# Performance work log

Measured on AMD Instinct MI355X. Metric: run time of the kernel, lower is better.

Reference implementation:

```python
import math
import jax, jax.numpy as jnp
import numpy as np

WS = 4            # window size
LS = 2 * WS       # local context size
NH = 8            # num heads
DIM = 128
EPS = 1e-5


def setup_inputs() -> dict:
    key = jax.random.key(0)
    ks = jax.random.split(key, 8)
    B, C, H, W = 4, DIM, 48, 48
    features = jax.random.normal(ks[0], (B, C, H, W), dtype=jnp.float32)
    s = 0.02
    return {
        'features': features,
        'ln_w': jnp.ones((C,), jnp.float32),
        'ln_b': jnp.zeros((C,), jnp.float32),
        'q_w': jax.random.normal(ks[1], (C, C), jnp.float32) * s,
        'q_b': jnp.zeros((C,), jnp.float32),
        'kv_w': jax.random.normal(ks[2], (2 * C, C), jnp.float32) * s,
        'kv_b': jnp.zeros((2 * C,), jnp.float32),
        'out_w': jax.random.normal(ks[3], (C, C), jnp.float32) * s,
        'out_b': jnp.zeros((C,), jnp.float32),
    }


def _avgpool_tokens(x, k):
    # x: [B,C,H,W] -> [B, (H//k)*(W//k), C]
    B, C, H, W = x.shape
    t = x.reshape(B, C, H // k, k, W // k, k).mean(axis=(3, 5))
    return t.reshape(B, C, -1).transpose(0, 2, 1)


def reference(features, ln_w, ln_b, q_w, q_b, kv_w, kv_b, out_w, out_b):
    B, C, H, W = features.shape
    Hw, Ww = H // WS, W // WS
    nw = Hw * Ww
    hd = C // NH

    # ---- window partition: [B,C,H,W] -> [B*nw, WS*WS, C]
    qt = features.reshape(B, C, Hw, WS, Ww, WS).transpose(0, 2, 4, 3, 5, 1)
    qt = qt.reshape(B * nw, WS * WS, C)

    # ---- LayerNorm(dim)
    mu = qt.mean(-1, keepdims=True)
    var = qt.var(-1, keepdims=True)
    qt = (qt - mu) / jnp.sqrt(var + EPS) * ln_w + ln_b

    # ---- local context: pad to target, unfold kernel=LS stride=WS
    target = (int(math.sqrt(nw)) - 1) * WS + LS
    ph, pw = max(0, target - H), max(0, target - W)
    pad = ((0, 0), (0, 0), (ph // 2, ph - ph // 2), (pw // 2, pw - pw // 2))
    padded = jnp.pad(features, pad)
    # channel order of patches is (C, kh, kw), same as torch unfold
    patches = jax.lax.conv_general_dilated_patches(
        padded, filter_shape=(LS, LS), window_strides=(WS, WS), padding='VALID')
    local = patches.reshape(B, C, LS * LS, nw).transpose(0, 3, 2, 1)
    local = local.reshape(B * nw, LS * LS, C)

    # ---- multi-scale pooled tokens, broadcast to each window
    mid = _avgpool_tokens(features, 2)      # [B, M, C]
    glo = _avgpool_tokens(features, 4)      # [B, G, C]
    mid = jnp.broadcast_to(mid[:, None], (B, nw) + mid.shape[1:]).reshape(B * nw, -1, C)
    glo = jnp.broadcast_to(glo[:, None], (B, nw) + glo.shape[1:]).reshape(B * nw, -1, C)

    kv_tokens = jnp.concatenate([local, mid, glo], axis=1)  # [B*nw, Nkv, C]

    # ---- projections (torch Linear: x @ W.T + b)
    queries = qt @ q_w.T + q_b
    kv = kv_tokens @ kv_w.T + kv_b
    keys, values = kv[..., :C], kv[..., C:]

    # ---- multi-head attention
    Nq, Nkv = queries.shape[1], keys.shape[1]
    q = queries.reshape(-1, Nq, NH, hd)
    k = keys.reshape(-1, Nkv, NH, hd)
    v = values.reshape(-1, Nkv, NH, hd)
    scores = jnp.einsum('bqhd,bkhd->bhqk', q, k) / math.sqrt(hd)
    weights = jax.nn.softmax(scores, axis=-1)
    attended = jnp.einsum('bhqk,bkhd->bqhd', weights, v).reshape(-1, Nq, C)

    out = attended @ out_w.T + out_b

    # ---- window reconstruction -> [B,C,H,W]
    out = out.reshape(B, Hw, Ww, WS, WS, C).transpose(0, 5, 1, 3, 2, 4)
    out = out.reshape(B, C, H, W)
    return out + features
```

## Files before the change

kernel.cpp:

```cpp
#include <hip/hip_runtime.h>


typedef unsigned short u16;
typedef short v8s __attribute__((ext_vector_type(8)));
typedef v8s __attribute__((may_alias)) v8s_am;
typedef short v4s __attribute__((ext_vector_type(4)));
typedef v4s __attribute__((may_alias)) v4s_am;
typedef float v4f __attribute__((ext_vector_type(4)));

#define MFMA_BF16(a, b, c) __builtin_amdgcn_mfma_f32_16x16x32_bf16(a, b, c, 0, 0, 0)

#if __has_builtin(__builtin_amdgcn_mfma_f32_16x16x16bf16_1k)
#define MFMA16(a, b, c) __builtin_amdgcn_mfma_f32_16x16x16bf16_1k(a, b, c, 0, 0, 0)
#else
static __device__ __forceinline__ v4f mfma16_fb(v4s a, v4s b, v4f c) {
    v8s a8 = {a[0], a[1], a[2], a[3], 0, 0, 0, 0};
    v8s b8 = {b[0], b[1], b[2], b[3], 0, 0, 0, 0};
    return MFMA_BF16(a8, b8, c);
}
#define MFMA16(a, b, c) mfma16_fb(a, b, c)
#endif

#if __has_builtin(__builtin_amdgcn_exp2f)
#define EXP2(x) __builtin_amdgcn_exp2f(x)
#else
#define EXP2(x) exp2f(x)
#endif

__device__ __forceinline__ float b2f(u16 u) {
    union { unsigned int i; float f; } x;
    x.i = ((unsigned int)u) << 16;
    return x.f;
}
__device__ __forceinline__ u16 f2b(float f) {
    union { float f; unsigned int i; } x;
    x.f = f;
    unsigned int u = x.i;
    return (u16)((u + 0x7fffu + ((u >> 16) & 1u)) >> 16);
}

__global__ __launch_bounds__(256) void k_prep(
    const float* __restrict__ F,
    const float* __restrict__ qw, const float* __restrict__ kvw,
    const float* __restrict__ ow,
    const float* __restrict__ lnw, const float* __restrict__ lnb,
    u16* __restrict__ Xt, u16* __restrict__ Wb, float* __restrict__ MuRs,
    u16* __restrict__ Pml)
{
    int blk = blockIdx.x;
    int t = threadIdx.x;
    if (blk >= 304) {
        int gid = (blk - 304) * 256 + t;
        int row = gid >> 4;
        int seg = gid & 15;
        v8s outv;
        if (row < 2304) {
            int b = row / 576, r = row % 576;
            int i = r / 24, j = r % 24;
#pragma unroll
            for (int jc = 0; jc < 8; ++jc) {
                int c = seg * 8 + jc;
                const float* src = F + ((size_t)(b * 128 + c)) * 2304 + (2 * i) * 48 + 2 * j;
                float2 a = *(const float2*)src;
                float2 d = *(const float2*)(src + 48);
                outv[jc] = (short)f2b((a.x + a.y + d.x + d.y) * 0.25f);
            }
        } else {
            int r2 = row - 2304;
            int b = r2 / 144, r = r2 % 144;
            int i = r / 12, j = r % 12;
#pragma unroll
            for (int jc = 0; jc < 8; ++jc) {
                int c = seg * 8 + jc;
                const float* src = F + ((size_t)(b * 128 + c)) * 2304 + (4 * i) * 48 + 4 * j;
                float s = 0.f;
#pragma unroll
                for (int di = 0; di < 4; ++di) {
                    float4 v = *(const float4*)(src + di * 48);
                    s += (v.x + v.y) + (v.z + v.w);
                }
                outv[jc] = (short)f2b(s * 0.0625f);
            }
        }
        *(v8s_am*)&Pml[((size_t)row) * 128 + seg * 8] = outv;
        return;
    }
    if (blk >= 288) {
        int base = (blk - 288) * 4096 + t * 16;
#pragma unroll
        for (int i = 0; i < 4; ++i) {
            int idx = base + i * 4;
            const float* src; int off;
            if (idx < 16384)      { src = qw;  off = idx; }
            else if (idx < 49152) { src = kvw; off = idx - 16384; }
            else                  { src = ow;  off = idx - 49152; }
            float4 v = *(const float4*)(src + off);
            unsigned long long packed =
                (unsigned long long)f2b(v.x) |
                ((unsigned long long)f2b(v.y) << 16) |
                ((unsigned long long)f2b(v.z) << 32) |
                ((unsigned long long)f2b(v.w) << 48);
            *(unsigned long long*)(Wb + idx) = packed;
        }
        if (blk == 288) {
            Wb[65536 + t] = f2b(t < 128 ? lnw[t] : lnb[t - 128]);
        }
        return;
    }
    __shared__ u16 X[128][34];
    int b = blk / 72;
    int p0 = (blk % 72) * 32;
#pragma unroll 4
    for (int i = 0; i < 16; ++i) {
        int c = i * 8 + (t >> 5);
        int pix = t & 31;
        X[c][pix] = f2b(F[((size_t)(b * 128 + c)) * 2304 + p0 + pix]);
    }
    __syncthreads();
    int pix = t >> 3;
    int c0 = (t & 7) * 16;
    size_t row = (size_t)(b * 2304 + p0 + pix) * 128;
    float s = 0.f, s2 = 0.f;
#pragma unroll
    for (int sg = 0; sg < 2; ++sg) {
        v8s raw;
#pragma unroll
        for (int j = 0; j < 8; ++j) {
            u16 u = X[c0 + sg * 8 + j][pix];
            raw[j] = (short)u;
            float v = b2f(u);
            s += v; s2 += v * v;
        }
        *(v8s_am*)&Xt[row + c0 + sg * 8] = raw;
    }
    s += __shfl_xor(s, 1);  s2 += __shfl_xor(s2, 1);
    s += __shfl_xor(s, 2);  s2 += __shfl_xor(s2, 2);
    s += __shfl_xor(s, 4);  s2 += __shfl_xor(s2, 4);
    if ((t & 7) == 0) {
        float mean = s * (1.f / 128.f);
        float var = s2 * (1.f / 128.f) - mean * mean;
        float rstd = rsqrtf(var + 1e-5f);
        MuRs[(b * 2304 + p0 + pix) * 2]     = mean;
        MuRs[(b * 2304 + p0 + pix) * 2 + 1] = rstd;
    }
}

__global__ __launch_bounds__(256) void k_gemm_kv(
    const u16* __restrict__ Pml,
    const u16* __restrict__ W,
    const float* __restrict__ bias,
    u16* __restrict__ KVg,
    u16* __restrict__ VTg)
{
    __shared__ u16 Al[64][136];
    __shared__ u16 Wl[64][136];
    int tm = blockIdx.x * 64, tn = blockIdx.y * 64;
    int t = threadIdx.x;
    {
        int seg = t & 15, r0 = t >> 4;
#pragma unroll
        for (int i = 0; i < 4; ++i) {
            int r = r0 + 16 * i;
            *(v8s_am*)&Al[r][seg * 8] = *(const v8s_am*)&Pml[((size_t)(tm + r)) * 128 + seg * 8];
            *(v8s_am*)&Wl[r][seg * 8] = *(const v8s_am*)&W[((size_t)(tn + r)) * 128 + seg * 8];
        }
    }
    __syncthreads();
    int lane = t & 63, wave = t >> 6;
    int n15 = lane & 15, quad = lane >> 4;
    int wm = (wave & 1) * 32, wn = (wave >> 1) * 32;
    v4f acc[2][2] = {};
#pragma unroll
    for (int kc = 0; kc < 4; ++kc) {
        v8s a[2], bb[2];
#pragma unroll
        for (int im = 0; im < 2; ++im)
            a[im] = *(const v8s_am*)&Al[wm + im * 16 + n15][kc * 32 + quad * 8];
#pragma unroll
        for (int in = 0; in < 2; ++in)
            bb[in] = *(const v8s_am*)&Wl[wn + in * 16 + n15][kc * 32 + quad * 8];
#pragma unroll
        for (int im = 0; im < 2; ++im)
#pragma unroll
            for (int in = 0; in < 2; ++in)
                acc[im][in] = MFMA_BF16(a[im], bb[in], acc[im][in]);
    }
#pragma unroll
    for (int in = 0; in < 2; ++in) {
        int n = tn + wn + in * 16 + n15;
        float bv = bias[n];
#pragma unroll
        for (int im = 0; im < 2; ++im) {
            int mbase = tm + wm + im * 16 + quad * 4;
#pragma unroll
            for (int r = 0; r < 4; ++r) {
                int m = mbase + r;
                u16 h = f2b(acc[im][in][r] + bv);
                if (n < 128) {
                    KVg[((size_t)m) * 128 + n] = h;
                } else {
                    int ch = n - 128, bb2, tok;
                    if (m < 2304) { bb2 = m / 576; tok = m % 576; }
                    else { int r2 = m - 2304; bb2 = r2 / 144; tok = 576 + r2 % 144; }
                    VTg[((size_t)(bb2 * 128 + ch)) * 720 + tok] = h;
                }
            }
        }
    }
}

__global__ __launch_bounds__(512, 4) void k_attn_fused(
    const float* __restrict__ F,
    const u16* __restrict__ Xt,
    const float* __restrict__ MuRs,
    const u16* __restrict__ KVg,
    const u16* __restrict__ VTg,
    const u16* __restrict__ Wb,
    const float* __restrict__ qb,
    const float* __restrict__ kvb,
    const float* __restrict__ ob,
    float* __restrict__ Out)
{
    __shared__ u16 KB[2][64][136];
    __shared__ u16 VtW[8][16][68];

    const u16* qwb  = Wb;
    const u16* kvwb = Wb + 16384;
    const u16* owb  = Wb + 49152;
    const u16* lnwb = Wb + 65536;
    const u16* lnbb = Wb + 65664;
    u16* Atp = &VtW[0][0][0];

    int blk = blockIdx.x;
    int xcd = blk & 7, jj = blk >> 3;
    int b = xcd >> 1;
    int wr = (xcd & 1) * 6 + jj / 12;
    int wc = jj % 12;

    int t = threadIdx.x;
    int lane = t & 63, wave = t >> 6, n15 = lane & 15, quad = lane >> 4;
    v8s zf8 = {};
    v4f zz4 = {0.f, 0.f, 0.f, 0.f};
    const float QSCALE = 0.25f * 1.44269504f;

    int qh = wr * 4 + (n15 >> 2), qw_ = wc * 4 + (n15 & 3);
    int qpix = b * 2304 + qh * 48 + qw_;
    float mu = MuRs[qpix * 2], rstd = MuRs[qpix * 2 + 1];
    v8s xln[4];
#pragma unroll
    for (int kc = 0; kc < 4; ++kc) {
        v8s x  = *(const v8s_am*)&Xt[(size_t)qpix * 128 + kc * 32 + quad * 8];
        v8s lw = *(const v8s_am*)&lnwb[kc * 32 + quad * 8];
        v8s lb = *(const v8s_am*)&lnbb[kc * 32 + quad * 8];
        v8s y;
#pragma unroll
        for (int j = 0; j < 8; ++j)
            y[j] = (short)f2b((b2f((u16)x[j]) - mu) * rstd * b2f((u16)lw[j]) + b2f((u16)lb[j]));
        xln[kc] = y;
    }

    v4s qf;
    {
        int n0 = wave * 16;
        v4f qacc = zz4;
#pragma unroll
        for (int kc = 0; kc < 4; ++kc) {
            v8s aw = *(const v8s_am*)&qwb[((size_t)(n0 + n15)) * 128 + kc * 32 + quad * 8];
            qacc = MFMA_BF16(aw, xln[kc], qacc);
        }
#pragma unroll
        for (int r = 0; r < 4; ++r)
            qf[r] = (short)f2b((qacc[r] + qb[n0 + quad * 4 + r]) * QSCALE);
    }

    v4s kfloc[4];
#pragma unroll
    for (int g = 0; g < 4; ++g) {
        int tl = g * 16 + n15;
        int fh = tl >> 3, fw = tl & 7;
        int hh = wr * 4 - 2 + fh, ww = wc * 4 - 2 + fw;
        bool valid = (hh >= 0 && hh < 48 && ww >= 0 && ww < 48);
        size_t arow = (size_t)(b * 2304 + hh * 48 + ww) * 128;
        v8s xb[4];
#pragma unroll
        for (int kc = 0; kc < 4; ++kc) {
            v8s v = zf8;
            if (valid) v = *(const v8s_am*)&Xt[arow + kc * 32 + quad * 8];
            xb[kc] = v;
        }
#pragma unroll
        for (int s = 0; s < 2; ++s) {
            int sbase = s * 128 + wave * 16;
            v4f acc = zz4;
#pragma unroll
            for (int kc = 0; kc < 4; ++kc) {
                v8s aw = *(const v8s_am*)&kvwb[((size_t)(sbase + n15)) * 128 + kc * 32 + quad * 8];
                acc = MFMA_BF16(aw, xb[kc], acc);
            }
            if (s == 0) {
                v4s k4;
#pragma unroll
                for (int r = 0; r < 4; ++r)
                    k4[r] = (short)f2b(acc[r] + kvb[sbase + quad * 4 + r]);
                kfloc[g] = k4;
            } else {
#pragma unroll
                for (int r = 0; r < 4; ++r)
                    VtW[wave][quad * 4 + r][g * 16 + n15] =
                        f2b(acc[r] + kvb[sbase + quad * 4 + r]);
            }
        }
    }

    v8s stg[2];
#pragma unroll
    for (int i = 0; i < 2; ++i) {
        int chunk = i * 512 + t;
        stg[i] = *(const v8s_am*)&KVg[((size_t)(b * 576 + (chunk >> 4))) * 128 + (chunk & 15) * 8];
    }

    v4f oacc = zz4;
    float ls = 0.f;
    const u16* VTb = VTg + (size_t)b * 92160;

    asm volatile("s_waitcnt lgkmcnt(0)" ::: "memory");
#pragma unroll
    for (int g = 0; g < 4; ++g) {
        v4f St = MFMA16(kfloc[g], qf, zz4);
        float p0 = EXP2(St[0]), p1 = EXP2(St[1]);
        float p2 = EXP2(St[2]), p3 = EXP2(St[3]);
        ls += (p0 + p1) + (p2 + p3);
        v4s pk = {(short)f2b(p0), (short)f2b(p1), (short)f2b(p2), (short)f2b(p3)};
        v4s vf = *(const v4s_am*)&VtW[wave][n15][g * 16 + quad * 4];
        oacc = MFMA16(vf, pk, oacc);
    }

#pragma unroll
    for (int i = 0; i < 2; ++i) {
        int chunk = i * 512 + t;
        *(v8s_am*)&KB[1][chunk >> 4][(chunk & 15) * 8] = stg[i];
    }
    __syncthreads();

    for (int tb = 0; tb <= 10; ++tb) {
        v4s vp[4];
        {
            const u16* vrow = VTb + (size_t)(wave * 16 + n15) * 720 + tb * 64 + quad * 4;
#pragma unroll
            for (int g = 0; g < 4; ++g)
                vp[g] = *(const v4s_am*)(vrow + g * 16);
        }
        int nt_ = tb + 1;
        int rowbase = (nt_ < 9) ? (b * 576 + nt_ * 64)
                                : (2304 + b * 144 + nt_ * 64 - 576);
        int nrows = (nt_ == 11) ? 16 : 64;
        bool sv[2];
#pragma unroll
        for (int i = 0; i < 2; ++i) {
            int chunk = i * 512 + t;
            int rr = chunk >> 4;
            sv[i] = rr < nrows;
            if (sv[i])
                stg[i] = *(const v8s_am*)&KVg[((size_t)(rowbase + rr)) * 128 + (chunk & 15) * 8];
        }
        const u16 (*KBc)[136] = KB[1 - (tb & 1)];
#pragma unroll
        for (int g = 0; g < 4; ++g) {
            v4s kf = *(const v4s_am*)&KBc[g * 16 + n15][wave * 16 + quad * 4];
            v4f St = MFMA16(kf, qf, zz4);
            float p0 = EXP2(St[0]), p1 = EXP2(St[1]);
            float p2 = EXP2(St[2]), p3 = EXP2(St[3]);
            ls += (p0 + p1) + (p2 + p3);
            v4s pk = {(short)f2b(p0), (short)f2b(p1), (short)f2b(p2), (short)f2b(p3)};
            oacc = MFMA16(vp[g], pk, oacc);
        }
#pragma unroll
        for (int i = 0; i < 2; ++i) {
            if (sv[i]) {
                int chunk = i * 512 + t;
                *(v8s_am*)&KB[tb & 1][chunk >> 4][(chunk & 15) * 8] = stg[i];
            }
        }
        __syncthreads();
    }
    {
        v4s vf = *(const v4s_am*)(VTb + (size_t)(wave * 16 + n15) * 720 + 704 + quad * 4);
        v4s kf = *(const v4s_am*)&KB[0][n15][wave * 16 + quad * 4];
        v4f St = MFMA16(kf, qf, zz4);
        float p0 = EXP2(St[0]), p1 = EXP2(St[1]);
        float p2 = EXP2(St[2]), p3 = EXP2(St[3]);
        ls += (p0 + p1) + (p2 + p3);
        v4s pk = {(short)f2b(p0), (short)f2b(p1), (short)f2b(p2), (short)f2b(p3)};
        oacc = MFMA16(vf, pk, oacc);
    }

    ls += __shfl_xor(ls, 16);
    ls += __shfl_xor(ls, 32);
    {
        float inv = 1.f / ls;
        v4s a4 = {(short)f2b(oacc[0] * inv), (short)f2b(oacc[1] * inv),
                  (short)f2b(oacc[2] * inv), (short)f2b(oacc[3] * inv)};
        *(v4s_am*)&Atp[n15 * 136 + wave * 16 + quad * 4] = a4;
    }
    __syncthreads();

    {
        int n0 = wave * 16;
        v4f oa = zz4;
#pragma unroll
        for (int kc = 0; kc < 4; ++kc) {
            v8s af = *(const v8s_am*)&Atp[n15 * 136 + kc * 32 + quad * 8];
            v8s bf = *(const v8s_am*)&owb[((size_t)(n0 + n15)) * 128 + kc * 32 + quad * 8];
            oa = MFMA_BF16(af, bf, oa);
        }
        int c = n0 + n15;
        float bv = ob[c];
#pragma unroll
        for (int r = 0; r < 4; ++r) {
            int pix = quad * 4 + r;
            int hh = wr * 4 + (pix >> 2), ww_ = wc * 4 + (pix & 3);
            size_t idx = ((size_t)(b * 128 + c)) * 2304 + hh * 48 + ww_;
            Out[idx] = oa[r] + bv + F[idx];
        }
    }
}

extern "C" void kernel_launch(void* const* d_in, const int* in_sizes, int n_in,
                              void* d_out, int out_size, void* d_ws, size_t ws_size,
                              hipStream_t stream)
{
    const float* F   = (const float*)d_in[0];
    const float* lnw = (const float*)d_in[1];
    const float* lnb = (const float*)d_in[2];
    const float* qw  = (const float*)d_in[3];
    const float* qb  = (const float*)d_in[4];
    const float* kvw = (const float*)d_in[5];
    const float* kvb = (const float*)d_in[6];
    const float* ow  = (const float*)d_in[7];
    const float* ob  = (const float*)d_in[8];
    float* Out = (float*)d_out;

    u16* ws    = (u16*)d_ws;
    u16* Xt    = ws;
    u16* Pml   = Xt + 9216 * 128;
    u16* KVg   = Pml + 2880 * 128;
    u16* VTg   = KVg + 2880 * 128;
    u16* Wb    = VTg + 4 * 128 * 720;
    float* MuRs = (float*)(Wb + 65792);
    u16* kvwb = Wb + 16384;

    k_prep<<<484, 256, 0, stream>>>(F, qw, kvw, ow, lnw, lnb, Xt, Wb, MuRs, Pml);
    k_gemm_kv<<<dim3(45, 4), 256, 0, stream>>>(Pml, kvwb, kvb, KVg, VTg);
    k_attn_fused<<<576, 512, 0, stream>>>(F, Xt, MuRs, KVg, VTg, Wb,
                                          qb, kvb, ob, Out);
}
```

Baseline: 135.1 us.

## Fuse pooling into KV GEMM, stage V transpose via LDS, drop K LDS buffering

The average pooling of mid/global tokens moves out of the prep kernel and into the KV GEMM, which reads the bf16 transposed features (Xt) instead of a separate pooled buffer, so one kernel's work and one intermediate round trip go away. V outputs of the mid-scale tiles are transposed through LDS so VTg gets vectorised, coalesced stores. The attention kernel stops double-buffering K tiles in shared memory with per-tile barriers and instead loads K and V fragments straight from global memory, which lowers LDS use and removes syncs but adds strided global loads that depend on cache hits. Pooling now runs on bf16-rounded features, which can change numerics slightly.

```diff
diff --git a/kernel.cpp b/kernel.cpp
--- a/kernel.cpp
+++ b/kernel.cpp
@@ -44,47 +44,10 @@
     const float* __restrict__ qw, const float* __restrict__ kvw,
     const float* __restrict__ ow,
     const float* __restrict__ lnw, const float* __restrict__ lnb,
-    u16* __restrict__ Xt, u16* __restrict__ Wb, float* __restrict__ MuRs,
-    u16* __restrict__ Pml)
+    u16* __restrict__ Xt, u16* __restrict__ Wb, float* __restrict__ MuRs)
 {
     int blk = blockIdx.x;
     int t = threadIdx.x;
-    if (blk >= 304) {
-        int gid = (blk - 304) * 256 + t;
-        int row = gid >> 4;
-        int seg = gid & 15;
-        v8s outv;
-        if (row < 2304) {
-            int b = row / 576, r = row % 576;
-            int i = r / 24, j = r % 24;
-#pragma unroll
-            for (int jc = 0; jc < 8; ++jc) {
-                int c = seg * 8 + jc;
-                const float* src = F + ((size_t)(b * 128 + c)) * 2304 + (2 * i) * 48 + 2 * j;
-                float2 a = *(const float2*)src;
-                float2 d = *(const float2*)(src + 48);
-                outv[jc] = (short)f2b((a.x + a.y + d.x + d.y) * 0.25f);
-            }
-        } else {
-            int r2 = row - 2304;
-            int b = r2 / 144, r = r2 % 144;
-            int i = r / 12, j = r % 12;
-#pragma unroll
-            for (int jc = 0; jc < 8; ++jc) {
-                int c = seg * 8 + jc;
-                const float* src = F + ((size_t)(b * 128 + c)) * 2304 + (4 * i) * 48 + 4 * j;
-                float s = 0.f;
-#pragma unroll
-                for (int di = 0; di < 4; ++di) {
-                    float4 v = *(const float4*)(src + di * 48);
-                    s += (v.x + v.y) + (v.z + v.w);
-                }
-                outv[jc] = (short)f2b(s * 0.0625f);
-            }
-        }
-        *(v8s_am*)&Pml[((size_t)row) * 128 + seg * 8] = outv;
-        return;
-    }
     if (blk >= 288) {
         int base = (blk - 288) * 4096 + t * 16;
 #pragma unroll
@@ -146,7 +109,7 @@
 }
 
 __global__ __launch_bounds__(256) void k_gemm_kv(
-    const u16* __restrict__ Pml,
+    const u16* __restrict__ Xt,
     const u16* __restrict__ W,
     const float* __restrict__ bias,
     u16* __restrict__ KVg,
@@ -161,8 +124,59 @@
 #pragma unroll
         for (int i = 0; i < 4; ++i) {
             int r = r0 + 16 * i;
-            *(v8s_am*)&Al[r][seg * 8] = *(const v8s_am*)&Pml[((size_t)(tm + r)) * 128 + seg * 8];
             *(v8s_am*)&Wl[r][seg * 8] = *(const v8s_am*)&W[((size_t)(tn + r)) * 128 + seg * 8];
+        }
+    }
+    {
+        int r = t >> 2;
+        int cp = (t & 3) * 32;
+        int m = tm + r;
+        float s[32];
+#pragma unroll
+        for (int j = 0; j < 32; ++j) s[j] = 0.f;
+        if (m < 2304) {
+            int b = m / 576, loc = m % 576;
+            int i = loc / 24, j = loc % 24;
+            int base = b * 2304 + (2 * i) * 48 + 2 * j;
+#pragma unroll
+            for (int rr = 0; rr < 4; ++rr) {
+                int row = base + (rr >> 1) * 48 + (rr & 1);
+#pragma unroll
+                for (int k = 0; k < 4; ++k) {
+                    v8s x = *(const v8s_am*)&Xt[(size_t)row * 128 + cp + k * 8];
+#pragma unroll
+                    for (int jj = 0; jj < 8; ++jj) s[k * 8 + jj] += b2f((u16)x[jj]);
+                }
+            }
+#pragma unroll
+            for (int k = 0; k < 4; ++k) {
+                v8s o;
+#pragma unroll
+                for (int jj = 0; jj < 8; ++jj) o[jj] = (short)f2b(s[k * 8 + jj] * 0.25f);
+                *(v8s_am*)&Al[r][cp + k * 8] = o;
+            }
+        } else {
+            int r2 = m - 2304;
+            int b = r2 / 144, loc = r2 % 144;
+            int i = loc / 12, j = loc % 12;
+            int base = b * 2304 + (4 * i) * 48 + 4 * j;
+#pragma unroll
+            for (int rr = 0; rr < 16; ++rr) {
+                int row = base + (rr >> 2) * 48 + (rr & 3);
+#pragma unroll
+                for (int k = 0; k < 4; ++k) {
+                    v8s x = *(const v8s_am*)&Xt[(size_t)row * 128 + cp + k * 8];
+#pragma unroll
+                    for (int jj = 0; jj < 8; ++jj) s[k * 8 + jj] += b2f((u16)x[jj]);
+                }
+            }
+#pragma unroll
+            for (int k = 0; k < 4; ++k) {
+                v8s o;
+#pragma unroll
+                for (int jj = 0; jj < 8; ++jj) o[jj] = (short)f2b(s[k * 8 + jj] * 0.0625f);
+                *(v8s_am*)&Al[r][cp + k * 8] = o;
+            }
         }
     }
     __syncthreads();
@@ -185,6 +199,10 @@
             for (int in = 0; in < 2; ++in)
                 acc[im][in] = MFMA_BF16(a[im], bb[in], acc[im][in]);
     }
+    bool vblk = (tn >= 128);
+    bool vfast = vblk && (tm < 2304);
+    u16* vt = &Al[0][0];
+    if (vfast) __syncthreads();
 #pragma unroll
     for (int in = 0; in < 2; ++in) {
         int n = tn + wn + in * 16 + n15;
@@ -196,17 +214,32 @@
             for (int r = 0; r < 4; ++r) {
                 int m = mbase + r;
                 u16 h = f2b(acc[im][in][r] + bv);
-                if (n < 128) {
+                if (!vblk) {
                     KVg[((size_t)m) * 128 + n] = h;
+                } else if (vfast) {
+                    vt[(n - tn) * 72 + (wm + im * 16 + quad * 4 + r)] = h;
                 } else {
                     int ch = n - 128, bb2, tok;
-                    if (m < 2304) { bb2 = m / 576; tok = m % 576; }
-                    else { int r2 = m - 2304; bb2 = r2 / 144; tok = 576 + r2 % 144; }
+                    int r2 = m - 2304; bb2 = r2 / 144; tok = 576 + r2 % 144;
                     VTg[((size_t)(bb2 * 128 + ch)) * 720 + tok] = h;
                 }
             }
         }
     }
+    if (vfast) {
+        __syncthreads();
+        int ch = t >> 2, seg = t & 3;
+        int b = tm / 576, tokbase = tm % 576;
+        v8s a0 = *(const v8s_am*)&vt[ch * 72 + seg * 16];
+        v8s a1 = *(const v8s_am*)&vt[ch * 72 + seg * 16 + 8];
+        size_t d = ((size_t)(b * 128 + (tn - 128) + ch)) * 720 + tokbase + seg * 16;
+        *(v8s_am*)&VTg[d]     = a0;
+        *(v8s_am*)&VTg[d + 8] = a1;
+    }
+}
+
+__device__ __forceinline__ int rbase_of(int b, int tb) {
+    return (tb < 9) ? (b * 576 + tb * 64) : (2304 + b * 144 + (tb - 9) * 64);
 }
 
 __global__ __launch_bounds__(512, 4) void k_attn_fused(
@@ -221,15 +254,14 @@
     const float* __restrict__ ob,
     float* __restrict__ Out)
 {
-    __shared__ u16 KB[2][64][136];
     __shared__ u16 VtW[8][16][68];
+    __shared__ u16 At[16][136];
 
     const u16* qwb  = Wb;
     const u16* kvwb = Wb + 16384;
     const u16* owb  = Wb + 49152;
     const u16* lnwb = Wb + 65536;
     const u16* lnbb = Wb + 65664;
-    u16* Atp = &VtW[0][0][0];
 
     int blk = blockIdx.x;
     int xcd = blk & 7, jj = blk >> 3;
@@ -312,18 +344,11 @@
         }
     }
 
-    v8s stg[2];
-#pragma unroll
-    for (int i = 0; i < 2; ++i) {
-        int chunk = i * 512 + t;
-        stg[i] = *(const v8s_am*)&KVg[((size_t)(b * 576 + (chunk >> 4))) * 128 + (chunk & 15) * 8];
-    }
-
     v4f oacc = zz4;
     float ls = 0.f;
-    const u16* VTb = VTg + (size_t)b * 92160;
 
     asm volatile("s_waitcnt lgkmcnt(0)" ::: "memory");
+    __builtin_amdgcn_sched_barrier(0);
 #pragma unroll
     for (int g = 0; g < 4; ++g) {
         v4f St = MFMA16(kfloc[g], qf, zz4);
@@ -335,57 +360,31 @@
         oacc = MFMA16(vf, pk, oacc);
     }
 
-#pragma unroll
-    for (int i = 0; i < 2; ++i) {
-        int chunk = i * 512 + t;
-        *(v8s_am*)&KB[1][chunk >> 4][(chunk & 15) * 8] = stg[i];
-    }
-    __syncthreads();
-
-    for (int tb = 0; tb <= 10; ++tb) {
-        v4s vp[4];
-        {
-            const u16* vrow = VTb + (size_t)(wave * 16 + n15) * 720 + tb * 64 + quad * 4;
-#pragma unroll
-            for (int g = 0; g < 4; ++g)
-                vp[g] = *(const v4s_am*)(vrow + g * 16);
-        }
-        int nt_ = tb + 1;
-        int rowbase = (nt_ < 9) ? (b * 576 + nt_ * 64)
-                                : (2304 + b * 144 + nt_ * 64 - 576);
-        int nrows = (nt_ == 11) ? 16 : 64;
-        bool sv[2];
-#pragma unroll
-        for (int i = 0; i < 2; ++i) {
-            int chunk = i * 512 + t;
-            int rr = chunk >> 4;
-            sv[i] = rr < nrows;
-            if (sv[i])
-                stg[i] = *(const v8s_am*)&KVg[((size_t)(rowbase + rr)) * 128 + (chunk & 15) * 8];
-        }
-        const u16 (*KBc)[136] = KB[1 - (tb & 1)];
+    const u16* kcol  = KVg + wave * 16 + quad * 4;
+    const u16* vrow0 = VTg + (size_t)b * 92160 + (size_t)(wave * 16 + n15) * 720 + quad * 4;
+#pragma unroll
+    for (int tb = 0; tb < 11; ++tb) {
+        int rbase = rbase_of(b, tb);
+        v4s kf[4], vp[4];
 #pragma unroll
         for (int g = 0; g < 4; ++g) {
-            v4s kf = *(const v4s_am*)&KBc[g * 16 + n15][wave * 16 + quad * 4];
-            v4f St = MFMA16(kf, qf, zz4);
+            kf[g] = *(const v4s_am*)(kcol + (size_t)(rbase + g * 16 + n15) * 128);
+            vp[g] = *(const v4s_am*)(vrow0 + tb * 64 + g * 16);
+        }
+#pragma unroll
+        for (int g = 0; g < 4; ++g) {
+            v4f St = MFMA16(kf[g], qf, zz4);
             float p0 = EXP2(St[0]), p1 = EXP2(St[1]);
             float p2 = EXP2(St[2]), p3 = EXP2(St[3]);
             ls += (p0 + p1) + (p2 + p3);
             v4s pk = {(short)f2b(p0), (short)f2b(p1), (short)f2b(p2), (short)f2b(p3)};
             oacc = MFMA16(vp[g], pk, oacc);
         }
-#pragma unroll
-        for (int i = 0; i < 2; ++i) {
-            if (sv[i]) {
-                int chunk = i * 512 + t;
-                *(v8s_am*)&KB[tb & 1][chunk >> 4][(chunk & 15) * 8] = stg[i];
-            }
-        }
-        __syncthreads();
-    }
-    {
-        v4s vf = *(const v4s_am*)(VTb + (size_t)(wave * 16 + n15) * 720 + 704 + quad * 4);
-        v4s kf = *(const v4s_am*)&KB[0][n15][wave * 16 + quad * 4];
+    }
+    {
+        int rbase = 2304 + b * 144 + 128;
+        v4s kf = *(const v4s_am*)(kcol + (size_t)(rbase + n15) * 128);
+        v4s vf = *(const v4s_am*)(vrow0 + 704);
         v4f St = MFMA16(kf, qf, zz4);
         float p0 = EXP2(St[0]), p1 = EXP2(St[1]);
         float p2 = EXP2(St[2]), p3 = EXP2(St[3]);
@@ -400,7 +399,7 @@
         float inv = 1.f / ls;
         v4s a4 = {(short)f2b(oacc[0] * inv), (short)f2b(oacc[1] * inv),
                   (short)f2b(oacc[2] * inv), (short)f2b(oacc[3] * inv)};
-        *(v4s_am*)&Atp[n15 * 136 + wave * 16 + quad * 4] = a4;
+        *(v4s_am*)&At[n15][wave * 16 + quad * 4] = a4;
     }
     __syncthreads();
 
@@ -409,7 +408,7 @@
         v4f oa = zz4;
 #pragma unroll
         for (int kc = 0; kc < 4; ++kc) {
-            v8s af = *(const v8s_am*)&Atp[n15 * 136 + kc * 32 + quad * 8];
+            v8s af = *(const v8s_am*)&At[n15][kc * 32 + quad * 8];
             v8s bf = *(const v8s_am*)&owb[((size_t)(n0 + n15)) * 128 + kc * 32 + quad * 8];
             oa = MFMA_BF16(af, bf, oa);
         }
@@ -449,8 +448,8 @@
     float* MuRs = (float*)(Wb + 65792);
     u16* kvwb = Wb + 16384;
 
-    k_prep<<<484, 256, 0, stream>>>(F, qw, kvw, ow, lnw, lnb, Xt, Wb, MuRs, Pml);
-    k_gemm_kv<<<dim3(45, 4), 256, 0, stream>>>(Pml, kvwb, kvb, KVg, VTg);
+    k_prep<<<304, 256, 0, stream>>>(F, qw, kvw, ow, lnw, lnb, Xt, Wb, MuRs);
+    k_gemm_kv<<<dim3(45, 4), 256, 0, stream>>>(Xt, kvwb, kvb, KVg, VTg);
     k_attn_fused<<<576, 512, 0, stream>>>(F, Xt, MuRs, KVg, VTg, Wb,
                                           qb, kvb, ob, Out);
 }
```

Result: slower. 151.6 us (+12.2%).

## Fuse pooling into KV GEMM prep kernel and process two windows per attention block

Applied to the files above, without the earlier changes.

Merges the pooled-token computation and the KV projection GEMM into the prep kernel. The GEMM blocks now pool features directly into shared memory and convert kv weights on the fly, which removes the Pml round trip and one launch. V-transpose writes for the mid tokens are staged through LDS so they go out as coalesced stores. The attention kernel now handles two adjacent windows per block (288 blocks), so each loaded shared K/V tile serves two query sets, at the cost of more registers and fewer blocks.

```diff
diff --git a/kernel.cpp b/kernel.cpp
--- a/kernel.cpp
+++ b/kernel.cpp
@@ -39,50 +39,136 @@
     return (u16)((u + 0x7fffu + ((u >> 16) & 1u)) >> 16);
 }
 
-__global__ __launch_bounds__(256) void k_prep(
+__global__ __launch_bounds__(256) void k_prep_gemm(
     const float* __restrict__ F,
     const float* __restrict__ qw, const float* __restrict__ kvw,
     const float* __restrict__ ow,
     const float* __restrict__ lnw, const float* __restrict__ lnb,
+    const float* __restrict__ kvb,
     u16* __restrict__ Xt, u16* __restrict__ Wb, float* __restrict__ MuRs,
-    u16* __restrict__ Pml)
+    u16* __restrict__ KVg, u16* __restrict__ VTg)
 {
+    __shared__ u16 SH[17408];
     int blk = blockIdx.x;
     int t = threadIdx.x;
+
     if (blk >= 304) {
-        int gid = (blk - 304) * 256 + t;
-        int row = gid >> 4;
-        int seg = gid & 15;
-        v8s outv;
-        if (row < 2304) {
-            int b = row / 576, r = row % 576;
-            int i = r / 24, j = r % 24;
-#pragma unroll
-            for (int jc = 0; jc < 8; ++jc) {
-                int c = seg * 8 + jc;
-                const float* src = F + ((size_t)(b * 128 + c)) * 2304 + (2 * i) * 48 + 2 * j;
-                float2 a = *(const float2*)src;
-                float2 d = *(const float2*)(src + 48);
-                outv[jc] = (short)f2b((a.x + a.y + d.x + d.y) * 0.25f);
-            }
-        } else {
-            int r2 = row - 2304;
-            int b = r2 / 144, r = r2 % 144;
-            int i = r / 12, j = r % 12;
-#pragma unroll
-            for (int jc = 0; jc < 8; ++jc) {
-                int c = seg * 8 + jc;
-                const float* src = F + ((size_t)(b * 128 + c)) * 2304 + (4 * i) * 48 + 4 * j;
-                float s = 0.f;
-#pragma unroll
-                for (int di = 0; di < 4; ++di) {
-                    float4 v = *(const float4*)(src + di * 48);
-                    s += (v.x + v.y) + (v.z + v.w);
+        u16 (*Al)[136] = (u16(*)[136])SH;
+        u16 (*Wl)[136] = (u16(*)[136])(SH + 8704);
+        int gb = blk - 304;
+        int tm = (gb % 45) * 64, tn = (gb / 45) * 64;
+        {
+            int seg = t & 15, r0 = t >> 4;
+#pragma unroll
+            for (int i = 0; i < 4; ++i) {
+                int r = r0 + 16 * i;
+                const float* src = kvw + (size_t)(tn + r) * 128 + seg * 8;
+                float4 v0 = *(const float4*)src;
+                float4 v1 = *(const float4*)(src + 4);
+                v8s o = {(short)f2b(v0.x), (short)f2b(v0.y), (short)f2b(v0.z), (short)f2b(v0.w),
+                         (short)f2b(v1.x), (short)f2b(v1.y), (short)f2b(v1.z), (short)f2b(v1.w)};
+                *(v8s_am*)&Wl[r][seg * 8] = o;
+            }
+        }
+        {
+            int rs = t >> 2;
+            int cp = (t & 3) * 32;
+            int m = tm + rs;
+            float s[32];
+            if (m < 2304) {
+                int bb = m / 576, loc = m % 576;
+                int ii = loc / 24, jj2 = loc % 24;
+                const float* f0 = F + (size_t)(bb * 128 + cp) * 2304 + (2 * ii) * 48 + 2 * jj2;
+#pragma unroll
+                for (int cc = 0; cc < 32; ++cc) {
+                    const float* src = f0 + (size_t)cc * 2304;
+                    float2 a = *(const float2*)src;
+                    float2 d = *(const float2*)(src + 48);
+                    s[cc] = (a.x + a.y + d.x + d.y) * 0.25f;
                 }
-                outv[jc] = (short)f2b(s * 0.0625f);
-            }
-        }
-        *(v8s_am*)&Pml[((size_t)row) * 128 + seg * 8] = outv;
+            } else {
+                int r2 = m - 2304;
+                int bb = r2 / 144, loc = r2 % 144;
+                int ii = loc / 12, jj2 = loc % 12;
+                const float* f0 = F + (size_t)(bb * 128 + cp) * 2304 + (4 * ii) * 48 + 4 * jj2;
+#pragma unroll
+                for (int cc = 0; cc < 32; ++cc) {
+                    const float* src = f0 + (size_t)cc * 2304;
+                    float ss = 0.f;
+#pragma unroll
+                    for (int di = 0; di < 4; ++di) {
+                        float4 v = *(const float4*)(src + di * 48);
+                        ss += (v.x + v.y) + (v.z + v.w);
+                    }
+                    s[cc] = ss * 0.0625f;
+                }
+            }
+#pragma unroll
+            for (int k = 0; k < 4; ++k) {
+                v8s o;
+#pragma unroll
+                for (int jj = 0; jj < 8; ++jj) o[jj] = (short)f2b(s[k * 8 + jj]);
+                *(v8s_am*)&Al[rs][cp + k * 8] = o;
+            }
+        }
+        __syncthreads();
+        int lane = t & 63, wave = t >> 6;
+        int n15 = lane & 15, quad = lane >> 4;
+        int wm = (wave & 1) * 32, wn = (wave >> 1) * 32;
+        v4f acc[2][2] = {};
+#pragma unroll
+        for (int kc = 0; kc < 4; ++kc) {
+            v8s a[2], bb[2];
+#pragma unroll
+            for (int im = 0; im < 2; ++im)
+                a[im] = *(const v8s_am*)&Al[wm + im * 16 + n15][kc * 32 + quad * 8];
+#pragma unroll
+            for (int in = 0; in < 2; ++in)
+                bb[in] = *(const v8s_am*)&Wl[wn + in * 16 + n15][kc * 32 + quad * 8];
+#pragma unroll
+            for (int im = 0; im < 2; ++im)
+#pragma unroll
+                for (int in = 0; in < 2; ++in)
+                    acc[im][in] = MFMA_BF16(a[im], bb[in], acc[im][in]);
+        }
+        bool vblk = (tn >= 128);
+        bool vfast = vblk && (tm < 2304);
+        u16* vt = &Al[0][0];
+        if (vfast) __syncthreads();
+#pragma unroll
+        for (int in = 0; in < 2; ++in) {
+            int n = tn + wn + in * 16 + n15;
+            float bv = kvb[n];
+#pragma unroll
+            for (int im = 0; im < 2; ++im) {
+                int mbase = tm + wm + im * 16 + quad * 4;
+#pragma unroll
+                for (int r = 0; r < 4; ++r) {
+                    int m = mbase + r;
+                    u16 h = f2b(acc[im][in][r] + bv);
+                    if (!vblk) {
+                        KVg[((size_t)m) * 128 + n] = h;
+                    } else if (vfast) {
+                        vt[(n - tn) * 72 + (wm + im * 16 + quad * 4 + r)] = h;
+                    } else {
+                        int ch = n - 128;
+                        int r2 = m - 2304;
+                        int bb2 = r2 / 144, tok = 576 + r2 % 144;
+                        VTg[((size_t)(bb2 * 128 + ch)) * 720 + tok] = h;
+                    }
+                }
+            }
+        }
+        if (vfast) {
+            __syncthreads();
+            int ch = t >> 2, seg = t & 3;
+            int bb2 = tm / 576, tokbase = tm % 576;
+            v8s a0 = *(const v8s_am*)&vt[ch * 72 + seg * 16];
+            v8s a1 = *(const v8s_am*)&vt[ch * 72 + seg * 16 + 8];
+            size_t d = ((size_t)(bb2 * 128 + (tn - 128) + ch)) * 720 + tokbase + seg * 16;
+            *(v8s_am*)&VTg[d]     = a0;
+            *(v8s_am*)&VTg[d + 8] = a1;
+        }
         return;
     }
     if (blk >= 288) {
@@ -107,7 +193,7 @@
         }
         return;
     }
-    __shared__ u16 X[128][34];
+    u16 (*X)[34] = (u16(*)[34])SH;
     int b = blk / 72;
     int p0 = (blk % 72) * 32;
 #pragma unroll 4
@@ -142,70 +228,6 @@
         float rstd = rsqrtf(var + 1e-5f);
         MuRs[(b * 2304 + p0 + pix) * 2]     = mean;
         MuRs[(b * 2304 + p0 + pix) * 2 + 1] = rstd;
-    }
-}
-
-__global__ __launch_bounds__(256) void k_gemm_kv(
-    const u16* __restrict__ Pml,
-    const u16* __restrict__ W,
-    const float* __restrict__ bias,
-    u16* __restrict__ KVg,
-    u16* __restrict__ VTg)
-{
-    __shared__ u16 Al[64][136];
-    __shared__ u16 Wl[64][136];
-    int tm = blockIdx.x * 64, tn = blockIdx.y * 64;
-    int t = threadIdx.x;
-    {
-        int seg = t & 15, r0 = t >> 4;
-#pragma unroll
-        for (int i = 0; i < 4; ++i) {
-            int r = r0 + 16 * i;
-            *(v8s_am*)&Al[r][seg * 8] = *(const v8s_am*)&Pml[((size_t)(tm + r)) * 128 + seg * 8];
-            *(v8s_am*)&Wl[r][seg * 8] = *(const v8s_am*)&W[((size_t)(tn + r)) * 128 + seg * 8];
-        }
-    }
-    __syncthreads();
-    int lane = t & 63, wave = t >> 6;
-    int n15 = lane & 15, quad = lane >> 4;
-    int wm = (wave & 1) * 32, wn = (wave >> 1) * 32;
-    v4f acc[2][2] = {};
-#pragma unroll
-    for (int kc = 0; kc < 4; ++kc) {
-        v8s a[2], bb[2];
-#pragma unroll
-        for (int im = 0; im < 2; ++im)
-            a[im] = *(const v8s_am*)&Al[wm + im * 16 + n15][kc * 32 + quad * 8];
-#pragma unroll
-        for (int in = 0; in < 2; ++in)
-            bb[in] = *(const v8s_am*)&Wl[wn + in * 16 + n15][kc * 32 + quad * 8];
-#pragma unroll
-        for (int im = 0; im < 2; ++im)
-#pragma unroll
-            for (int in = 0; in < 2; ++in)
-                acc[im][in] = MFMA_BF16(a[im], bb[in], acc[im][in]);
-    }
-#pragma unroll
-    for (int in = 0; in < 2; ++in) {
-        int n = tn + wn + in * 16 + n15;
-        float bv = bias[n];
-#pragma unroll
-        for (int im = 0; im < 2; ++im) {
-            int mbase = tm + wm + im * 16 + quad * 4;
-#pragma unroll
-            for (int r = 0; r < 4; ++r) {
-                int m = mbase + r;
-                u16 h = f2b(acc[im][in][r] + bv);
-                if (n < 128) {
-                    KVg[((size_t)m) * 128 + n] = h;
-                } else {
-                    int ch = n - 128, bb2, tok;
-                    if (m < 2304) { bb2 = m / 576; tok = m % 576; }
-                    else { int r2 = m - 2304; bb2 = r2 / 144; tok = 576 + r2 % 144; }
-                    VTg[((size_t)(bb2 * 128 + ch)) * 720 + tok] = h;
-                }
-            }
-        }
     }
 }
 
@@ -222,20 +244,20 @@
     float* __restrict__ Out)
 {
     __shared__ u16 KB[2][64][136];
-    __shared__ u16 VtW[8][16][68];
+    __shared__ u16 VtW[8][2][16][68];
 
     const u16* qwb  = Wb;
     const u16* kvwb = Wb + 16384;
     const u16* owb  = Wb + 49152;
     const u16* lnwb = Wb + 65536;
     const u16* lnbb = Wb + 65664;
-    u16* Atp = &VtW[0][0][0];
+    u16* Atp = &VtW[0][0][0][0];
 
     int blk = blockIdx.x;
     int xcd = blk & 7, jj = blk >> 3;
     int b = xcd >> 1;
-    int wr = (xcd & 1) * 6 + jj / 12;
-    int wc = jj % 12;
+    int wr = (xcd & 1) * 6 + jj / 6;
+    int wcp = jj % 6;
 
     int t = threadIdx.x;
     int lane = t & 63, wave = t >> 6, n15 = lane & 15, quad = lane >> 4;
@@ -243,24 +265,32 @@
     v4f zz4 = {0.f, 0.f, 0.f, 0.f};
     const float QSCALE = 0.25f * 1.44269504f;
 
-    int qh = wr * 4 + (n15 >> 2), qw_ = wc * 4 + (n15 & 3);
-    int qpix = b * 2304 + qh * 48 + qw_;
-    float mu = MuRs[qpix * 2], rstd = MuRs[qpix * 2 + 1];
-    v8s xln[4];
-#pragma unroll
-    for (int kc = 0; kc < 4; ++kc) {
-        v8s x  = *(const v8s_am*)&Xt[(size_t)qpix * 128 + kc * 32 + quad * 8];
-        v8s lw = *(const v8s_am*)&lnwb[kc * 32 + quad * 8];
-        v8s lb = *(const v8s_am*)&lnbb[kc * 32 + quad * 8];
-        v8s y;
-#pragma unroll
-        for (int j = 0; j < 8; ++j)
-            y[j] = (short)f2b((b2f((u16)x[j]) - mu) * rstd * b2f((u16)lw[j]) + b2f((u16)lb[j]));
-        xln[kc] = y;
-    }
-
-    v4s qf;
-    {
+    v8s stg[2];
+#pragma unroll
+    for (int i = 0; i < 2; ++i) {
+        int chunk = i * 512 + t;
+        stg[i] = *(const v8s_am*)&KVg[((size_t)(b * 576 + (chunk >> 4))) * 128 + (chunk & 15) * 8];
+    }
+
+    v4s qf[2];
+#pragma unroll
+    for (int wi = 0; wi < 2; ++wi) {
+        int wc = wcp * 2 + wi;
+        int qh = wr * 4 + (n15 >> 2), qw_ = wc * 4 + (n15 & 3);
+        int qpix = b * 2304 + qh * 48 + qw_;
+        float mu = MuRs[qpix * 2], rstd = MuRs[qpix * 2 + 1];
+        v8s xln[4];
+#pragma unroll
+        for (int kc = 0; kc < 4; ++kc) {
+            v8s x  = *(const v8s_am*)&Xt[(size_t)qpix * 128 + kc * 32 + quad * 8];
+            v8s lw = *(const v8s_am*)&lnwb[kc * 32 + quad * 8];
+            v8s lb = *(const v8s_am*)&lnbb[kc * 32 + quad * 8];
+            v8s y;
+#pragma unroll
+            for (int j = 0; j < 8; ++j)
+                y[j] = (short)f2b((b2f((u16)x[j]) - mu) * rstd * b2f((u16)lw[j]) + b2f((u16)lb[j]));
+            xln[kc] = y;
+        }
         int n0 = wave * 16;
         v4f qacc = zz4;
 #pragma unroll
@@ -268,71 +298,74 @@
             v8s aw = *(const v8s_am*)&qwb[((size_t)(n0 + n15)) * 128 + kc * 32 + quad * 8];
             qacc = MFMA_BF16(aw, xln[kc], qacc);
         }
+        v4s q4;
 #pragma unroll
         for (int r = 0; r < 4; ++r)
-            qf[r] = (short)f2b((qacc[r] + qb[n0 + quad * 4 + r]) * QSCALE);
-    }
-
-    v4s kfloc[4];
-#pragma unroll
-    for (int g = 0; g < 4; ++g) {
-        int tl = g * 16 + n15;
-        int fh = tl >> 3, fw = tl & 7;
-        int hh = wr * 4 - 2 + fh, ww = wc * 4 - 2 + fw;
-        bool valid = (hh >= 0 && hh < 48 && ww >= 0 && ww < 48);
-        size_t arow = (size_t)(b * 2304 + hh * 48 + ww) * 128;
-        v8s xb[4];
-#pragma unroll
-        for (int kc = 0; kc < 4; ++kc) {
-            v8s v = zf8;
-            if (valid) v = *(const v8s_am*)&Xt[arow + kc * 32 + quad * 8];
-            xb[kc] = v;
-        }
-#pragma unroll
-        for (int s = 0; s < 2; ++s) {
-            int sbase = s * 128 + wave * 16;
-            v4f acc = zz4;
+            q4[r] = (short)f2b((qacc[r] + qb[n0 + quad * 4 + r]) * QSCALE);
+        qf[wi] = q4;
+    }
+
+    v4s kfloc[2][4];
+#pragma unroll
+    for (int wi = 0; wi < 2; ++wi) {
+        int wc = wcp * 2 + wi;
+#pragma unroll
+        for (int g = 0; g < 4; ++g) {
+            int tl = g * 16 + n15;
+            int fh = tl >> 3, fw = tl & 7;
+            int hh = wr * 4 - 2 + fh, ww = wc * 4 - 2 + fw;
+            bool valid = (hh >= 0 && hh < 48 && ww >= 0 && ww < 48);
+            size_t arow = (size_t)(b * 2304 + hh * 48 + ww) * 128;
+            v8s xb[4];
 #pragma unroll
             for (int kc = 0; kc < 4; ++kc) {
-                v8s aw = *(const v8s_am*)&kvwb[((size_t)(sbase + n15)) * 128 + kc * 32 + quad * 8];
-                acc = MFMA_BF16(aw, xb[kc], acc);
-            }
-            if (s == 0) {
-                v4s k4;
-#pragma unroll
-                for (int r = 0; r < 4; ++r)
-                    k4[r] = (short)f2b(acc[r] + kvb[sbase + quad * 4 + r]);
-                kfloc[g] = k4;
-            } else {
-#pragma unroll
-                for (int r = 0; r < 4; ++r)
-                    VtW[wave][quad * 4 + r][g * 16 + n15] =
-                        f2b(acc[r] + kvb[sbase + quad * 4 + r]);
-            }
-        }
-    }
-
-    v8s stg[2];
-#pragma unroll
-    for (int i = 0; i < 2; ++i) {
-        int chunk = i * 512 + t;
-        stg[i] = *(const v8s_am*)&KVg[((size_t)(b * 576 + (chunk >> 4))) * 128 + (chunk & 15) * 8];
-    }
-
-    v4f oacc = zz4;
-    float ls = 0.f;
+                v8s v = zf8;
+                if (valid) v = *(const v8s_am*)&Xt[arow + kc * 32 + quad * 8];
+                xb[kc] = v;
+            }
+#pragma unroll
+            for (int s = 0; s < 2; ++s) {
+                int sbase = s * 128 + wave * 16;
+                v4f acc = zz4;
+#pragma unroll
+                for (int kc = 0; kc < 4; ++kc) {
+                    v8s aw = *(const v8s_am*)&kvwb[((size_t)(sbase + n15)) * 128 + kc * 32 + quad * 8];
+                    acc = MFMA_BF16(aw, xb[kc], acc);
+                }
+                if (s == 0) {
+                    v4s k4;
+#pragma unroll
+                    for (int r = 0; r < 4; ++r)
+                        k4[r] = (short)f2b(acc[r] + kvb[sbase + quad * 4 + r]);
+                    kfloc[wi][g] = k4;
+                } else {
+#pragma unroll
+                    for (int r = 0; r < 4; ++r)
+                        VtW[wave][wi][quad * 4 + r][g * 16 + n15] =
+                            f2b(acc[r] + kvb[sbase + quad * 4 + r]);
+                }
+            }
+        }
+    }
+
+    v4f oacc[2] = {};
+    float ls0 = 0.f, ls1 = 0.f;
     const u16* VTb = VTg + (size_t)b * 92160;
 
     asm volatile("s_waitcnt lgkmcnt(0)" ::: "memory");
 #pragma unroll
-    for (int g = 0; g < 4; ++g) {
-        v4f St = MFMA16(kfloc[g], qf, zz4);
-        float p0 = EXP2(St[0]), p1 = EXP2(St[1]);
-        float p2 = EXP2(St[2]), p3 = EXP2(St[3]);
-        ls += (p0 + p1) + (p2 + p3);
-        v4s pk = {(short)f2b(p0), (short)f2b(p1), (short)f2b(p2), (short)f2b(p3)};
-        v4s vf = *(const v4s_am*)&VtW[wave][n15][g * 16 + quad * 4];
-        oacc = MFMA16(vf, pk, oacc);
+    for (int wi = 0; wi < 2; ++wi) {
+#pragma unroll
+        for (int g = 0; g < 4; ++g) {
+            v4f St = MFMA16(kfloc[wi][g], qf[wi], zz4);
+            float p0 = EXP2(St[0]), p1 = EXP2(St[1]);
+            float p2 = EXP2(St[2]), p3 = EXP2(St[3]);
+            if (wi == 0) ls0 += (p0 + p1) + (p2 + p3);
+            else         ls1 += (p0 + p1) + (p2 + p3);
+            v4s pk = {(short)f2b(p0), (short)f2b(p1), (short)f2b(p2), (short)f2b(p3)};
+            v4s vf = *(const v4s_am*)&VtW[wave][wi][n15][g * 16 + quad * 4];
+            oacc[wi] = MFMA16(vf, pk, oacc[wi]);
+        }
     }
 
 #pragma unroll
@@ -367,12 +400,16 @@
 #pragma unroll
         for (int g = 0; g < 4; ++g) {
             v4s kf = *(const v4s_am*)&KBc[g * 16 + n15][wave * 16 + quad * 4];
-            v4f St = MFMA16(kf, qf, zz4);
-            float p0 = EXP2(St[0]), p1 = EXP2(St[1]);
-            float p2 = EXP2(St[2]), p3 = EXP2(St[3]);
-            ls += (p0 + p1) + (p2 + p3);
-            v4s pk = {(short)f2b(p0), (short)f2b(p1), (short)f2b(p2), (short)f2b(p3)};
-            oacc = MFMA16(vp[g], pk, oacc);
+            v4f St0 = MFMA16(kf, qf[0], zz4);
+            v4f St1 = MFMA16(kf, qf[1], zz4);
+            float a0 = EXP2(St0[0]), a1 = EXP2(St0[1]), a2 = EXP2(St0[2]), a3 = EXP2(St0[3]);
+            float b0 = EXP2(St1[0]), b1 = EXP2(St1[1]), b2 = EXP2(St1[2]), b3 = EXP2(St1[3]);
+            ls0 += (a0 + a1) + (a2 + a3);
+            ls1 += (b0 + b1) + (b2 + b3);
+            v4s pk0 = {(short)f2b(a0), (short)f2b(a1), (short)f2b(a2), (short)f2b(a3)};
+            v4s pk1 = {(short)f2b(b0), (short)f2b(b1), (short)f2b(b2), (short)f2b(b3)};
+            oacc[0] = MFMA16(vp[g], pk0, oacc[0]);
+            oacc[1] = MFMA16(vp[g], pk1, oacc[1]);
         }
 #pragma unroll
         for (int i = 0; i < 2; ++i) {
@@ -386,30 +423,38 @@
     {
         v4s vf = *(const v4s_am*)(VTb + (size_t)(wave * 16 + n15) * 720 + 704 + quad * 4);
         v4s kf = *(const v4s_am*)&KB[0][n15][wave * 16 + quad * 4];
-        v4f St = MFMA16(kf, qf, zz4);
-        float p0 = EXP2(St[0]), p1 = EXP2(St[1]);
-        float p2 = EXP2(St[2]), p3 = EXP2(St[3]);
-        ls += (p0 + p1) + (p2 + p3);
-        v4s pk = {(short)f2b(p0), (short)f2b(p1), (short)f2b(p2), (short)f2b(p3)};
-        oacc = MFMA16(vf, pk, oacc);
-    }
-
-    ls += __shfl_xor(ls, 16);
-    ls += __shfl_xor(ls, 32);
-    {
+        v4f St0 = MFMA16(kf, qf[0], zz4);
+        v4f St1 = MFMA16(kf, qf[1], zz4);
+        float a0 = EXP2(St0[0]), a1 = EXP2(St0[1]), a2 = EXP2(St0[2]), a3 = EXP2(St0[3]);
+        float b0 = EXP2(St1[0]), b1 = EXP2(St1[1]), b2 = EXP2(St1[2]), b3 = EXP2(St1[3]);
+        ls0 += (a0 + a1) + (a2 + a3);
+        ls1 += (b0 + b1) + (b2 + b3);
+        v4s pk0 = {(short)f2b(a0), (short)f2b(a1), (short)f2b(a2), (short)f2b(a3)};
+        v4s pk1 = {(short)f2b(b0), (short)f2b(b1), (short)f2b(b2), (short)f2b(b3)};
+        oacc[0] = MFMA16(vf, pk0, oacc[0]);
+        oacc[1] = MFMA16(vf, pk1, oacc[1]);
+    }
+
+#pragma unroll
+    for (int wi = 0; wi < 2; ++wi) {
+        float ls = wi == 0 ? ls0 : ls1;
+        ls += __shfl_xor(ls, 16);
+        ls += __shfl_xor(ls, 32);
         float inv = 1.f / ls;
-        v4s a4 = {(short)f2b(oacc[0] * inv), (short)f2b(oacc[1] * inv),
-                  (short)f2b(oacc[2] * inv), (short)f2b(oacc[3] * inv)};
-        *(v4s_am*)&Atp[n15 * 136 + wave * 16 + quad * 4] = a4;
+        v4s a4 = {(short)f2b(oacc[wi][0] * inv), (short)f2b(oacc[wi][1] * inv),
+                  (short)f2b(oacc[wi][2] * inv), (short)f2b(oacc[wi][3] * inv)};
+        *(v4s_am*)&Atp[wi * 2176 + n15 * 136 + wave * 16 + quad * 4] = a4;
     }
     __syncthreads();
 
-    {
+#pragma unroll
+    for (int wi = 0; wi < 2; ++wi) {
+        int wc = wcp * 2 + wi;
         int n0 = wave * 16;
         v4f oa = zz4;
 #pragma unroll
         for (int kc = 0; kc < 4; ++kc) {
-            v8s af = *(const v8s_am*)&Atp[n15 * 136 + kc * 32 + quad * 8];
+            v8s af = *(const v8s_am*)&Atp[wi * 2176 + n15 * 136 + kc * 32 + quad * 8];
             v8s bf = *(const v8s_am*)&owb[((size_t)(n0 + n15)) * 128 + kc * 32 + quad * 8];
             oa = MFMA_BF16(af, bf, oa);
         }
@@ -447,10 +492,9 @@
     u16* VTg   = KVg + 2880 * 128;
     u16* Wb    = VTg + 4 * 128 * 720;
     float* MuRs = (float*)(Wb + 65792);
-    u16* kvwb = Wb + 16384;
-
-    k_prep<<<484, 256, 0, stream>>>(F, qw, kvw, ow, lnw, lnb, Xt, Wb, MuRs, Pml);
-    k_gemm_kv<<<dim3(45, 4), 256, 0, stream>>>(Pml, kvwb, kvb, KVg, VTg);
-    k_attn_fused<<<576, 512, 0, stream>>>(F, Xt, MuRs, KVg, VTg, Wb,
+
+    k_prep_gemm<<<484, 256, 0, stream>>>(F, qw, kvw, ow, lnw, lnb, kvb,
+                                         Xt, Wb, MuRs, KVg, VTg);
+    k_attn_fused<<<288, 512, 0, stream>>>(F, Xt, MuRs, KVg, VTg, Wb,
                                           qb, kvb, ob, Out);
 }
```

After: 139.6 us. 1.03x slower.
